# Kernel optimization log

Hardware: AMD Instinct MI355X
Metric: run time of the kernel (lower is better)

The kernel has to match this reference:

```python
import jax, jax.numpy as jnp
import numpy as np

B, T, N, F_IN, H, EV = 2, 12, 20000, 9, 64, 9
E = 200000


def setup_inputs() -> dict:
    key = jax.random.key(0)
    k = jax.random.split(key, 24)
    s = 0.1
    rn = lambda kk, shp: s * jax.random.normal(kk, shp, dtype=jnp.float32)
    d = {
        'graph_at_instance': jax.random.normal(k[0], (B, T, N, F_IN), dtype=jnp.float32),
        'target_event': jax.random.normal(k[1], (B, EV), dtype=jnp.float32),
        'input_event': jax.random.normal(k[2], (B, EV), dtype=jnp.float32),
        'edge_weight': jax.random.uniform(k[3], (E,), dtype=jnp.float32),
        'edge_src': jax.random.randint(k[4], (E,), 0, N, dtype=jnp.int32),
        'edge_dst': jax.random.randint(k[5], (E,), 0, N, dtype=jnp.int32),
        # 12 per-timestep GraphSAGE blocks (conv1: 9->64, conv2: 64->64, conv3: 64->9)
        'W1l': rn(k[6], (T, F_IN, H)), 'b1': jnp.zeros((T, H), jnp.float32), 'W1r': rn(k[7], (T, F_IN, H)),
        'W2l': rn(k[8], (T, H, H)),    'b2': jnp.zeros((T, H), jnp.float32), 'W2r': rn(k[9], (T, H, H)),
        'W3l': rn(k[10], (T, H, F_IN)),'b3': jnp.zeros((T, F_IN), jnp.float32), 'W3r': rn(k[11], (T, H, F_IN)),
        # 12 per-timestep GRU cells (9 -> 9), standard GRUCell parameterization
        'Wih': rn(k[12], (T, F_IN, 3 * F_IN)), 'Whh': rn(k[13], (T, F_IN, 3 * F_IN)),
        'bih': jnp.zeros((T, 3 * F_IN), jnp.float32), 'bhh': jnp.zeros((T, 3 * F_IN), jnp.float32),
        # encoder (18 -> 64) and decoder (64 -> 1)
        'enc_W': rn(k[14], (F_IN + EV, 64)), 'enc_b': jnp.zeros((64,), jnp.float32),
        'dec_W': rn(k[15], (64, 1)), 'dec_b': jnp.zeros((1,), jnp.float32),
    }
    return d


def _forward(graph_at_instance, target_event, input_event, edge_weight,
             W1l, b1, W1r, W2l, b2, W2r, W3l, b3, W3r,
             Wih, Whh, bih, bhh, enc_W, enc_b, dec_W, dec_b,
             edge_src, edge_dst):
    # in-degree for mean aggregation (clamped to avoid div by 0)
    deg = jnp.zeros((N,), jnp.float32).at[edge_dst].add(1.0)
    deg = jnp.maximum(deg, 1.0)[None, :, None]  # [1, N, 1]

    def sage(x, Wl, bl, Wr):
        # x: [B, N, d].  Weighted mean aggregation over edges, then lin_l(agg) + lin_r(x).
        m = x[:, edge_src] * edge_weight[None, :, None]          # [B, E, d]
        agg = jnp.zeros_like(x).at[:, edge_dst].add(m) / deg     # [B, N, d]
        return agg @ Wl + bl + x @ Wr

    def gru_cell(x, h, wih, whh, bih_t, bhh_t):
        gi = x @ wih + bih_t
        gh = h @ whh + bhh_t
        gir, giz, gin = jnp.split(gi, 3, axis=-1)
        ghr, ghz, ghn = jnp.split(gh, 3, axis=-1)
        r = jax.nn.sigmoid(gir + ghr)
        z = jax.nn.sigmoid(giz + ghz)
        n = jnp.tanh(gin + r * ghn)
        return (1.0 - z) * n + z * h

    def step(h, xs):
        xt, w1l, bb1, w1r, w2l, bb2, w2r, w3l, bb3, w3r, wih, whh, bih_t, bhh_t = xs
        x = jax.nn.elu(sage(xt, w1l, bb1, w1r))
        x = jax.nn.elu(sage(x, w2l, bb2, w2r))
        x = jax.nn.elu(sage(x, w3l, bb3, w3r))
        h = gru_cell(x, h, wih, whh, bih_t, bhh_t)
        return h, h

    xs = (jnp.swapaxes(graph_at_instance, 0, 1),  # [T, B, N, 9]
          W1l, b1, W1r, W2l, b2, W2r, W3l, b3, W3r, Wih, Whh, bih, bhh)
    h0 = jnp.zeros((B, N, F_IN), jnp.float32)
    _, outs = jax.lax.scan(step, h0, xs)          # [T, B, N, 9]
    outs = jnp.swapaxes(outs, 0, 1)               # [B, T, N, 9]

    te = jnp.broadcast_to(target_event[:, None, None, :], (B, T, N, EV))
    x = jnp.concatenate([outs, te], axis=-1)      # [B, T, N, 18]
    out = (x @ enc_W + enc_b) @ dec_W + dec_b     # [B, T, N, 1]
    mask = (graph_at_instance[..., 0:1] != 0).astype(out.dtype)
    return out * mask


def reference(graph_at_instance, target_event, input_event, edge_weight,
              W1l, b1, W1r, W2l, b2, W2r, W3l, b3, W3r,
              Wih, Whh, bih, bhh, enc_W, enc_b, dec_W, dec_b,
              edge_src, edge_dst):
    return _forward(graph_at_instance, target_event, input_event, edge_weight,
                    W1l, b1, W1r, W2l, b2, W2r, W3l, b3, W3r,
                    Wih, Whh, bih, bhh, enc_W, enc_b, dec_W, dec_b,
                    edge_src, edge_dst)
```

## Files before the change

### kernel.cpp

```cpp
#include <hip/hip_runtime.h>
#include <hip/hip_bf16.h>

#define BB 2
#define TT 12
#define NN 20000
#define FF 9
#define HH 64
#define EE 200000
#define NP 128

typedef __hip_bfloat16 bf;
typedef __attribute__((ext_vector_type(8))) short s8v;
typedef __attribute__((ext_vector_type(4))) float f4v;

__device__ unsigned g_xa[TT*NN*HH];
__device__ unsigned g_ag[TT*NN*HH];
__device__ unsigned g_xb[TT*NN*HH];
__device__ float2   g_x9[(size_t)NN*NP];
__device__ float2   g_xp[(size_t)NN*NP];
__device__ float2   g_z9[(size_t)NN*NP];
__device__ float2   g_r9[(size_t)NN*NP];
__device__ float2   g_a9[(size_t)NN*NP];
__device__ int      g_rp[NN+1];
__device__ int      g_cnt[NN];
__device__ int      g_csrc[EE];
__device__ float    g_cw[EE];
__device__ float    g_cvec[32];

__device__ __forceinline__ float lo2f(unsigned u){ unsigned v=u<<16; float f; __builtin_memcpy(&f,&v,4); return f; }
__device__ __forceinline__ float hi2f(unsigned u){ unsigned v=u&0xffff0000u; float f; __builtin_memcpy(&f,&v,4); return f; }
__device__ __forceinline__ unsigned short f2us(float f){ bf h=__float2bfloat16(f); unsigned short u; __builtin_memcpy(&u,&h,2); return u; }
__device__ __forceinline__ unsigned pack2(float a0, float a1){ return (unsigned)f2us(a0) | ((unsigned)f2us(a1)<<16); }
__device__ __forceinline__ float elu(float x){ return x>0.f ? x : expm1f(x); }

__global__ void k_zero(){
  int i = blockIdx.x*256 + threadIdx.x;
  if(i < NN) g_cnt[i] = 0;
}
__global__ void k_count(const int* __restrict__ dst){
  int e = blockIdx.x*256 + threadIdx.x;
  if(e < EE) atomicAdd(&g_cnt[dst[e]], 1);
}
__global__ void k_scan(){
  __shared__ int part[256];
  const int CH = 79;
  int t = threadIdx.x;
  int base = t*CH;
  int s = 0;
  for(int i=0;i<CH;i++){ int idx=base+i; if(idx<NN) s += g_cnt[idx]; }
  part[t] = s; __syncthreads();
  for(int off=1; off<256; off<<=1){
    int v = (t>=off) ? part[t-off] : 0;
    __syncthreads();
    part[t] += v;
    __syncthreads();
  }
  int run = (t==0) ? 0 : part[t-1];
  for(int i=0;i<CH;i++){
    int idx=base+i;
    if(idx<NN){ run += g_cnt[idx]; g_rp[idx+1] = run; }
  }
  if(t==0) g_rp[0] = 0;
}
__global__ void k_fill(const int* __restrict__ dst, const int* __restrict__ src,
                       const float* __restrict__ ew){
  int e = blockIdx.x*256 + threadIdx.x;
  if(e >= EE) return;
  int d = dst[e];
  int pos = g_rp[d] + atomicAdd(&g_cnt[d], 1);
  g_csrc[pos] = src[e];
  g_cw[pos]   = ew[e];
}

__global__ void k_head(const float* __restrict__ encW, const float* __restrict__ encb,
                       const float* __restrict__ decW, const float* __restrict__ decb,
                       const float* __restrict__ te){
  __shared__ float c[19];
  int tid = threadIdx.x;
  if(tid < 18){ float s=0.f; for(int j=0;j<64;j++) s += encW[tid*64+j]*decW[j]; c[tid]=s; }
  if(tid == 18){ float s=decb[0]; for(int j=0;j<64;j++) s += encb[j]*decW[j]; c[18]=s; }
  __syncthreads();
  if(tid < FF) g_cvec[tid] = c[tid];
  if(tid < BB){ float s=c[18]; for(int k=0;k<FF;k++) s += te[tid*FF+k]*c[9+k]; g_cvec[FF+tid]=s; }
}

__global__ void k_pack(const float* __restrict__ g){
  long i = (long)blockIdx.x*256 + threadIdx.x;
  if(i < (long)TT*NN*FF){
    int t = (int)(i / (NN*FF));
    int r = (int)(i - (long)t*NN*FF);
    int n = r / FF;
    int f = r - n*FF;
    float2 p;
    p.x = g[i];
    p.y = g[(long)TT*NN*FF + i];
    g_xp[(size_t)n*NP + t*FF + f] = p;
  }
}

__global__ void k_agg1(){
  int tid = threadIdx.x;
  int lane = tid & 63;
  int grp  = lane >> 4;
  int sub  = lane & 15;
  int wid = (blockIdx.x*256+tid)>>6, nw = gridDim.x*4;
  for(int n=wid; n<NN; n+=nw){
    int r0=g_rp[n], r1=g_rp[n+1];
    float inv = 1.f/fmaxf((float)(r1-r0), 1.f);
    float acc[16];
    #pragma unroll
    for(int s=0;s<16;s++) acc[s]=0.f;
    for(int base=r0; base<r1; base+=64){
      int cnt = min(64, r1-base);
      int ms = 0; float mw = 0.f;
      if(lane < cnt){ ms = g_csrc[base+lane]; mw = g_cw[base+lane]; }
      for(int k=0;k<cnt;k+=4){
        int   sg = __shfl(ms, k+grp, 64);
        float wg = __shfl(mw, k+grp, 64);
        const float4* p = reinterpret_cast<const float4*>(g_xp + (size_t)sg*NP) + sub*4;
        float4 v0=p[0], v1=p[1], v2=p[2], v3=p[3];
        acc[0]+=wg*v0.x; acc[1]+=wg*v0.y; acc[2]+=wg*v0.z; acc[3]+=wg*v0.w;
        acc[4]+=wg*v1.x; acc[5]+=wg*v1.y; acc[6]+=wg*v1.z; acc[7]+=wg*v1.w;
        acc[8]+=wg*v2.x; acc[9]+=wg*v2.y; acc[10]+=wg*v2.z; acc[11]+=wg*v2.w;
        acc[12]+=wg*v3.x; acc[13]+=wg*v3.y; acc[14]+=wg*v3.z; acc[15]+=wg*v3.w;
      }
    }
    #pragma unroll
    for(int s=0;s<16;s++){
      acc[s] += __shfl_xor(acc[s],16,64);
      acc[s] += __shfl_xor(acc[s],32,64);
    }
    if(grp == 0){
      float4* o = reinterpret_cast<float4*>(g_a9 + (size_t)n*NP) + sub*4;
      #pragma unroll
      for(int q=0;q<4;q++){
        float4 w;
        w.x = acc[q*4+0]*inv; w.y = acc[q*4+1]*inv;
        w.z = acc[q*4+2]*inv; w.w = acc[q*4+3]*inv;
        o[q] = w;
      }
    }
  }
}

__global__ __launch_bounds__(256) void k_gemm1(const float* __restrict__ Wl,
                                               const float* __restrict__ bias,
                                               const float* __restrict__ Wr){
  int t = blockIdx.y;
  __shared__ float sW[32*65];
  int tid = threadIdx.x;
  for(int i=tid; i<32*64; i+=256){
    int r = i >> 6, c = i & 63;
    float v = 0.f;
    if(r < FF)        v = Wl[(size_t)t*FF*HH + r*HH + c];
    else if(r < 2*FF) v = Wr[(size_t)t*FF*HH + (r-FF)*HH + c];
    sW[r*65+c] = v;
  }
  __syncthreads();
  int lane = tid & 63, wave = tid >> 6;
  int quad = lane >> 4, col = lane & 15;
  int base16 = blockIdx.x*64 + wave*16;
  if(base16 >= NN) return;
  size_t tb = (size_t)t*NN;
  int node = base16 + col;
  s8v A0, A1;
  #pragma unroll
  for(int j=0;j<8;j++){
    int k = quad*8 + j;
    float2 v = {0.f, 0.f};
    if(k < FF)        v = g_a9[(size_t)node*NP + t*FF + k];
    else if(k < 2*FF) v = g_xp[(size_t)node*NP + t*FF + (k-FF)];
    A0[j] = (short)f2us(v.x);
    A1[j] = (short)f2us(v.y);
  }
  #pragma unroll
  for(int nt=0; nt<4; nt++){
    f4v c0 = {0.f,0.f,0.f,0.f}, c1 = {0.f,0.f,0.f,0.f};
    s8v B;
    #pragma unroll
    for(int j=0;j<8;j++)
      B[j] = (short)f2us(sW[(quad*8+j)*65 + nt*16+col]);
    c0 = __builtin_amdgcn_mfma_f32_16x16x32_bf16(A0, B, c0, 0, 0, 0);
    c1 = __builtin_amdgcn_mfma_f32_16x16x32_bf16(A1, B, c1, 0, 0, 0);
    float bn = bias[t*HH + nt*16 + col];
    #pragma unroll
    for(int reg=0; reg<4; reg++){
      int nd = base16 + quad*4 + reg;
      g_xa[(tb+nd)*HH + nt*16 + col] = pack2(elu(c0[reg]+bn), elu(c1[reg]+bn));
    }
  }
}

__global__ void k_agg_all(){
  const unsigned* __restrict__ src = g_xa;
  int tid = threadIdx.x;
  int lane = tid & 63;
  int grp  = lane >> 4;
  int sub  = lane & 15;
  int wid = (blockIdx.x*256+tid)>>6, nw = gridDim.x*4;
  for(int idx=wid; idx<TT*NN; idx+=nw){
    unsigned ut = (unsigned)idx / NN;
    int n = idx - (int)(ut*NN);
    size_t tb = (size_t)ut*NN;
    const unsigned* __restrict__ rowp = src + tb*HH + (sub<<2);
    int r0=g_rp[n], r1=g_rp[n+1];
    float dg = fmaxf((float)(r1-r0), 1.f);
    float inv = 1.f/dg;
    float p0[4]={0.f,0.f,0.f,0.f}, p1[4]={0.f,0.f,0.f,0.f};
    for(int base=r0; base<r1; base+=64){
      int cnt = min(64, r1-base);
      int ms = 0; float mw = 0.f;
      if(lane < cnt){ ms = g_csrc[base+lane]; mw = g_cw[base+lane]; }
      for(int k=0;k<cnt;k+=4){
        int   sg = __shfl(ms, k+grp, 64);
        float wg = __shfl(mw, k+grp, 64);
        const uint4 v = *reinterpret_cast<const uint4*>(rowp + (size_t)sg*HH);
        p0[0]+=wg*lo2f(v.x); p1[0]+=wg*hi2f(v.x);
        p0[1]+=wg*lo2f(v.y); p1[1]+=wg*hi2f(v.y);
        p0[2]+=wg*lo2f(v.z); p1[2]+=wg*hi2f(v.z);
        p0[3]+=wg*lo2f(v.w); p1[3]+=wg*hi2f(v.w);
      }
    }
    #pragma unroll
    for(int q=0;q<4;q++){
      p0[q] += __shfl_xor(p0[q],16,64); p1[q] += __shfl_xor(p1[q],16,64);
      p0[q] += __shfl_xor(p0[q],32,64); p1[q] += __shfl_xor(p1[q],32,64);
    }
    if(lane < 16){
      uint4 o;
      o.x = pack2(p0[0]*inv, p1[0]*inv);
      o.y = pack2(p0[1]*inv, p1[1]*inv);
      o.z = pack2(p0[2]*inv, p1[2]*inv);
      o.w = pack2(p0[3]*inv, p1[3]*inv);
      *reinterpret_cast<uint4*>(g_ag + (tb + (size_t)n)*HH + (lane<<2)) = o;
    }
  }
}

__global__ __launch_bounds__(256) void k_gemm2_all(const float* __restrict__ Wl,
                                                   const float* __restrict__ bias,
                                                   const float* __restrict__ Wr){
  int t = blockIdx.y;
  __shared__ float sW[128*65];
  int tid = threadIdx.x;
  for(int i=tid; i<64*64; i+=256){
    int r = i >> 6, c = i & 63;
    sW[r*65+c]      = Wl[(size_t)t*4096 + i];
    sW[(r+64)*65+c] = Wr[(size_t)t*4096 + i];
  }
  __syncthreads();
  int lane = tid & 63, wave = tid >> 6;
  int quad = lane >> 4, col = lane & 15;
  int base16 = blockIdx.x*64 + wave*16;
  if(base16 >= NN) return;
  size_t tb = (size_t)t*NN;
  int nodeA = base16 + col;
  s8v A0[4], A1[4];
  #pragma unroll
  for(int ks=0; ks<4; ks++){
    const unsigned* srcb = (ks < 2) ? g_ag : g_xa;
    int koff = (ks & 1)*32 + quad*8;
    const uint4 u = *reinterpret_cast<const uint4*>(srcb + (tb+nodeA)*HH + koff);
    const uint4 v = *reinterpret_cast<const uint4*>(srcb + (tb+nodeA)*HH + koff + 4);
    unsigned uu[8] = {u.x,u.y,u.z,u.w,v.x,v.y,v.z,v.w};
    #pragma unroll
    for(int j=0;j<8;j++){
      A0[ks][j] = (short)(uu[j] & 0xffffu);
      A1[ks][j] = (short)(uu[j] >> 16);
    }
  }
  #pragma unroll
  for(int nt=0; nt<4; nt++){
    f4v c0 = {0.f,0.f,0.f,0.f}, c1 = {0.f,0.f,0.f,0.f};
    #pragma unroll
    for(int ks=0; ks<4; ks++){
      s8v B;
      #pragma unroll
      for(int j=0;j<8;j++)
        B[j] = (short)f2us(sW[(ks*32+quad*8+j)*65 + nt*16+col]);
      c0 = __builtin_amdgcn_mfma_f32_16x16x32_bf16(A0[ks], B, c0, 0, 0, 0);
      c1 = __builtin_amdgcn_mfma_f32_16x16x32_bf16(A1[ks], B, c1, 0, 0, 0);
    }
    float bn = bias[t*HH + nt*16 + col];
    #pragma unroll
    for(int reg=0; reg<4; reg++){
      int node = base16 + quad*4 + reg;
      g_xb[(tb+node)*HH + nt*16 + col] = pack2(elu(c0[reg]+bn), elu(c1[reg]+bn));
    }
  }
}

__global__ __launch_bounds__(256) void k_gemm3z(const float* __restrict__ Wl,
                                                const float* __restrict__ bias,
                                                const float* __restrict__ Wr){
  int t = blockIdx.y;
  __shared__ float sW[128*10];
  int tid = threadIdx.x;
  for(int i=tid; i<64*FF; i+=256){
    int r = i/FF, c = i - r*FF;
    sW[r*10+c]      = Wl[(size_t)t*HH*FF + i];
    sW[(r+64)*10+c] = Wr[(size_t)t*HH*FF + i];
  }
  __syncthreads();
  int lane = tid & 63, wave = tid >> 6;
  int quad = lane >> 4, col = lane & 15;
  int base16 = blockIdx.x*64 + wave*16;
  if(base16 >= NN) return;
  size_t tb = (size_t)t*NN;
  int nodeA = base16 + col;
  f4v z0={0.f,0.f,0.f,0.f}, z1={0.f,0.f,0.f,0.f};
  f4v r0={0.f,0.f,0.f,0.f}, r1={0.f,0.f,0.f,0.f};
  #pragma unroll
  for(int ks=0; ks<2; ks++){
    int koff = ks*32 + quad*8;
    const uint4 u = *reinterpret_cast<const uint4*>(g_xb + (tb+nodeA)*HH + koff);
    const uint4 v = *reinterpret_cast<const uint4*>(g_xb + (tb+nodeA)*HH + koff + 4);
    unsigned uu[8] = {u.x,u.y,u.z,u.w,v.x,v.y,v.z,v.w};
    s8v A0, A1, Bl, Br;
    #pragma unroll
    for(int j=0;j<8;j++){
      A0[j] = (short)(uu[j] & 0xffffu);
      A1[j] = (short)(uu[j] >> 16);
      int row = ks*32 + quad*8 + j;
      Bl[j] = (col < FF) ? (short)f2us(sW[row*10 + col])      : (short)0;
      Br[j] = (col < FF) ? (short)f2us(sW[(row+64)*10 + col]) : (short)0;
    }
    z0 = __builtin_amdgcn_mfma_f32_16x16x32_bf16(A0, Bl, z0, 0, 0, 0);
    z1 = __builtin_amdgcn_mfma_f32_16x16x32_bf16(A1, Bl, z1, 0, 0, 0);
    r0 = __builtin_amdgcn_mfma_f32_16x16x32_bf16(A0, Br, r0, 0, 0, 0);
    r1 = __builtin_amdgcn_mfma_f32_16x16x32_bf16(A1, Br, r1, 0, 0, 0);
  }
  if(col < FF){
    float bn = bias[t*FF + col];
    #pragma unroll
    for(int reg=0; reg<4; reg++){
      int node = base16 + quad*4 + reg;
      float2 oz; oz.x = z0[reg]; oz.y = z1[reg];
      float2 orr; orr.x = r0[reg]+bn; orr.y = r1[reg]+bn;
      g_z9[(size_t)node*NP + t*FF + col] = oz;
      g_r9[(size_t)node*NP + t*FF + col] = orr;
    }
  }
}

__global__ void k_agg9f(){
  int tid = threadIdx.x;
  int lane = tid & 63;
  int grp  = lane >> 4;
  int sub  = lane & 15;
  int wid = (blockIdx.x*256+tid)>>6, nw = gridDim.x*4;
  for(int n=wid; n<NN; n+=nw){
    int r0=g_rp[n], r1=g_rp[n+1];
    float inv = 1.f/fmaxf((float)(r1-r0), 1.f);
    float acc[16];
    #pragma unroll
    for(int s=0;s<16;s++) acc[s]=0.f;
    for(int base=r0; base<r1; base+=64){
      int cnt = min(64, r1-base);
      int ms = 0; float mw = 0.f;
      if(lane < cnt){ ms = g_csrc[base+lane]; mw = g_cw[base+lane]; }
      for(int k=0;k<cnt;k+=4){
        int   sg = __shfl(ms, k+grp, 64);
        float wg = __shfl(mw, k+grp, 64);
        const float4* p = reinterpret_cast<const float4*>(g_z9 + (size_t)sg*NP) + sub*4;
        float4 v0=p[0], v1=p[1], v2=p[2], v3=p[3];
        acc[0]+=wg*v0.x; acc[1]+=wg*v0.y; acc[2]+=wg*v0.z; acc[3]+=wg*v0.w;
        acc[4]+=wg*v1.x; acc[5]+=wg*v1.y; acc[6]+=wg*v1.z; acc[7]+=wg*v1.w;
        acc[8]+=wg*v2.x; acc[9]+=wg*v2.y; acc[10]+=wg*v2.z; acc[11]+=wg*v2.w;
        acc[12]+=wg*v3.x; acc[13]+=wg*v3.y; acc[14]+=wg*v3.z; acc[15]+=wg*v3.w;
      }
    }
    #pragma unroll
    for(int s=0;s<16;s++){
      acc[s] += __shfl_xor(acc[s],16,64);
      acc[s] += __shfl_xor(acc[s],32,64);
    }
    if(grp == 0){
      const float4* rp4 = reinterpret_cast<const float4*>(g_r9 + (size_t)n*NP) + sub*4;
      float4* o = reinterpret_cast<float4*>(g_x9 + (size_t)n*NP) + sub*4;
      #pragma unroll
      for(int q=0;q<4;q++){
        float4 r = rp4[q];
        float4 w;
        w.x = elu(acc[q*4+0]*inv + r.x);
        w.y = elu(acc[q*4+1]*inv + r.y);
        w.z = elu(acc[q*4+2]*inv + r.z);
        w.w = elu(acc[q*4+3]*inv + r.w);
        o[q] = w;
      }
    }
  }
}

__global__ __launch_bounds__(256) void k_gru_fused(const float* __restrict__ g,
                          const float* __restrict__ Wih, const float* __restrict__ Whh,
                          const float* __restrict__ bih, const float* __restrict__ bhh,
                          float* __restrict__ out){
  __shared__ float sWih[TT*FF*27];
  __shared__ float sWhh[TT*FF*27];
  __shared__ float sbih[TT*27], sbhh[TT*27];
  int tid = threadIdx.x;
  for(int i=tid;i<TT*FF*27;i+=256){ sWih[i]=Wih[i]; sWhh[i]=Whh[i]; }
  for(int i=tid;i<TT*27;i+=256){ sbih[i]=bih[i]; sbhh[i]=bhh[i]; }
  __syncthreads();
  int lane = tid & 63;
  int wv   = tid >> 6;
  int p    = lane / 9;
  int f    = lane - p*9;
  int gbase = p*9;
  int id = (blockIdx.x*4 + wv)*7 + p;
  bool valid = (p < 7) && (id < BB*NN);
  int b = 0, n = 0;
  if(valid){ b = (id >= NN) ? 1 : 0; n = id - b*NN; }
  float c9[FF];
  #pragma unroll
  for(int i=0;i<FF;i++) c9[i] = g_cvec[i];
  float cb = g_cvec[FF+b];
  float h = 0.f;
  float hs[FF];
  #pragma unroll
  for(int i=0;i<FF;i++) hs[i] = 0.f;
  for(int t=0;t<TT;t++){
    float x = 0.f;
    if(valid){
      float2 xf = g_x9[(size_t)n*NP + t*FF + f];
      x = b ? xf.y : xf.x;
    }
    float xs[FF];
    #pragma unroll
    for(int i=0;i<FF;i++) xs[i] = __shfl(x, gbase+i, 64);
    const float* wi = &sWih[t*FF*27];
    const float* wh = &sWhh[t*FF*27];
    float gir = sbih[t*27+f], giz = sbih[t*27+9+f], gin = sbih[t*27+18+f];
    float ghr = sbhh[t*27+f], ghz = sbhh[t*27+9+f], ghn = sbhh[t*27+18+f];
    #pragma unroll
    for(int i=0;i<FF;i++){
      float xi = xs[i], hi = hs[i];
      gir += xi*wi[i*27+f];    giz += xi*wi[i*27+9+f];    gin += xi*wi[i*27+18+f];
      ghr += hi*wh[i*27+f];    ghz += hi*wh[i*27+9+f];    ghn += hi*wh[i*27+18+f];
    }
    float r = 1.f/(1.f+__expf(-(gir+ghr)));
    float z = 1.f/(1.f+__expf(-(giz+ghz)));
    float nv = tanhf(gin + r*ghn);
    h = (1.f-z)*nv + z*h;
    #pragma unroll
    for(int i=0;i<FF;i++) hs[i] = __shfl(h, gbase+i, 64);
    if(valid && f == 0){
      float acc = cb;
      #pragma unroll
      for(int i=0;i<FF;i++) acc += hs[i]*c9[i];
      size_t gidx = (size_t)(b*TT+t)*NN + n;
      float m = (g[gidx*FF] != 0.f) ? 1.f : 0.f;
      out[gidx] = acc*m;
    }
  }
}

extern "C" void kernel_launch(void* const* d_in, const int* in_sizes, int n_in,
                              void* d_out, int out_size, void* d_ws, size_t ws_size,
                              hipStream_t stream){
  const float* g    = (const float*)d_in[0];
  const float* te   = (const float*)d_in[1];
  const float* ew   = (const float*)d_in[3];
  const int* esrc = (const int*)d_in[4];
  const int* edst = (const int*)d_in[5];
  const float* W1l=(const float*)d_in[6];  const float* b1 =(const float*)d_in[7];  const float* W1r=(const float*)d_in[8];
  const float* W2l=(const float*)d_in[9];  const float* b2 =(const float*)d_in[10]; const float* W2r=(const float*)d_in[11];
  const float* W3l=(const float*)d_in[12]; const float* b3 =(const float*)d_in[13]; const float* W3r=(const float*)d_in[14];
  const float* Wih=(const float*)d_in[15]; const float* Whh=(const float*)d_in[16];
  const float* bih=(const float*)d_in[17]; const float* bhh=(const float*)d_in[18];
  const float* encW=(const float*)d_in[19]; const float* encb=(const float*)d_in[20];
  const float* decW=(const float*)d_in[21]; const float* decb=(const float*)d_in[22];
  float* out = (float*)d_out;

  k_zero <<<(NN+255)/256, 256, 0, stream>>>();
  k_count<<<(EE+255)/256, 256, 0, stream>>>(edst);
  k_scan <<<1, 256, 0, stream>>>();
  k_zero <<<(NN+255)/256, 256, 0, stream>>>();
  k_fill <<<(EE+255)/256, 256, 0, stream>>>(edst, esrc, ew);
  k_head <<<1, 64, 0, stream>>>(encW, encb, decW, decb, te);
  k_pack <<<((long)TT*NN*FF+255)/256, 256, 0, stream>>>(g);

  dim3 ggm((NN+63)/64, TT);
  k_agg1<<<2048, 256, 0, stream>>>();
  k_gemm1<<<ggm, 256, 0, stream>>>(W1l, b1, W1r);
  k_agg_all<<<2048, 256, 0, stream>>>();
  k_gemm2_all<<<ggm, 256, 0, stream>>>(W2l, b2, W2r);
  k_gemm3z<<<ggm, 256, 0, stream>>>(W3l, b3, W3r);
  k_agg9f<<<2048, 256, 0, stream>>>();
  int nblk = (BB*NN + 27) / 28;
  k_gru_fused<<<nblk, 256, 0, stream>>>(g, Wih, Whh, bih, bhh, out);
}
```

Measured before the change: 540.0 us.

## Fuse conv2 and conv3 GEMMs via LDS, merge setup kernels, store bf16 weights

Combines the conv2 and conv3 GEMM kernels into one, keeping each wave's conv2 output tile in shared memory instead of writing and rereading a global intermediate buffer. The head-constant computation and the second count-zeroing are folded into the scan kernel, cutting three launches. Weights are converted to bf16 once when staged into shared memory rather than on every B-fragment read. The fused kernel uses more LDS per block (about 37 KB), which may reduce occupancy.

```diff
diff --git a/kernel.cpp b/kernel.cpp
--- a/kernel.cpp
+++ b/kernel.cpp
@@ -15,7 +15,6 @@
 
 __device__ unsigned g_xa[TT*NN*HH];
 __device__ unsigned g_ag[TT*NN*HH];
-__device__ unsigned g_xb[TT*NN*HH];
 __device__ float2   g_x9[(size_t)NN*NP];
 __device__ float2   g_xp[(size_t)NN*NP];
 __device__ float2   g_z9[(size_t)NN*NP];
@@ -41,8 +40,11 @@
   int e = blockIdx.x*256 + threadIdx.x;
   if(e < EE) atomicAdd(&g_cnt[dst[e]], 1);
 }
-__global__ void k_scan(){
+__global__ void k_scan(const float* __restrict__ encW, const float* __restrict__ encb,
+                       const float* __restrict__ decW, const float* __restrict__ decb,
+                       const float* __restrict__ te){
   __shared__ int part[256];
+  __shared__ float c[19];
   const int CH = 79;
   int t = threadIdx.x;
   int base = t*CH;
@@ -58,9 +60,14 @@
   int run = (t==0) ? 0 : part[t-1];
   for(int i=0;i<CH;i++){
     int idx=base+i;
-    if(idx<NN){ run += g_cnt[idx]; g_rp[idx+1] = run; }
+    if(idx<NN){ run += g_cnt[idx]; g_rp[idx+1] = run; g_cnt[idx] = 0; }
   }
   if(t==0) g_rp[0] = 0;
+  if(t < 18){ float v=0.f; for(int j=0;j<64;j++) v += encW[t*64+j]*decW[j]; c[t]=v; }
+  if(t == 18){ float v=decb[0]; for(int j=0;j<64;j++) v += encb[j]*decW[j]; c[18]=v; }
+  __syncthreads();
+  if(t < FF) g_cvec[t] = c[t];
+  if(t < BB){ float v=c[18]; for(int k=0;k<FF;k++) v += te[t*FF+k]*c[9+k]; g_cvec[FF+t]=v; }
 }
 __global__ void k_fill(const int* __restrict__ dst, const int* __restrict__ src,
                        const float* __restrict__ ew){
@@ -70,18 +77,6 @@
   int pos = g_rp[d] + atomicAdd(&g_cnt[d], 1);
   g_csrc[pos] = src[e];
   g_cw[pos]   = ew[e];
-}
-
-__global__ void k_head(const float* __restrict__ encW, const float* __restrict__ encb,
-                       const float* __restrict__ decW, const float* __restrict__ decb,
-                       const float* __restrict__ te){
-  __shared__ float c[19];
-  int tid = threadIdx.x;
-  if(tid < 18){ float s=0.f; for(int j=0;j<64;j++) s += encW[tid*64+j]*decW[j]; c[tid]=s; }
-  if(tid == 18){ float s=decb[0]; for(int j=0;j<64;j++) s += encb[j]*decW[j]; c[18]=s; }
-  __syncthreads();
-  if(tid < FF) g_cvec[tid] = c[tid];
-  if(tid < BB){ float s=c[18]; for(int k=0;k<FF;k++) s += te[tid*FF+k]*c[9+k]; g_cvec[FF+tid]=s; }
 }
 
 __global__ void k_pack(const float* __restrict__ g){
@@ -147,14 +142,14 @@
                                                const float* __restrict__ bias,
                                                const float* __restrict__ Wr){
   int t = blockIdx.y;
-  __shared__ float sW[32*65];
+  __shared__ unsigned short sW[32*65];
   int tid = threadIdx.x;
   for(int i=tid; i<32*64; i+=256){
     int r = i >> 6, c = i & 63;
     float v = 0.f;
     if(r < FF)        v = Wl[(size_t)t*FF*HH + r*HH + c];
     else if(r < 2*FF) v = Wr[(size_t)t*FF*HH + (r-FF)*HH + c];
-    sW[r*65+c] = v;
+    sW[r*65+c] = f2us(v);
   }
   __syncthreads();
   int lane = tid & 63, wave = tid >> 6;
@@ -179,7 +174,7 @@
     s8v B;
     #pragma unroll
     for(int j=0;j<8;j++)
-      B[j] = (short)f2us(sW[(quad*8+j)*65 + nt*16+col]);
+      B[j] = (short)sW[(quad*8+j)*65 + nt*16+col];
     c0 = __builtin_amdgcn_mfma_f32_16x16x32_bf16(A0, B, c0, 0, 0, 0);
     c1 = __builtin_amdgcn_mfma_f32_16x16x32_bf16(A1, B, c1, 0, 0, 0);
     float bn = bias[t*HH + nt*16 + col];
@@ -237,16 +232,26 @@
   }
 }
 
-__global__ __launch_bounds__(256) void k_gemm2_all(const float* __restrict__ Wl,
-                                                   const float* __restrict__ bias,
-                                                   const float* __restrict__ Wr){
+__global__ __launch_bounds__(256) void k_gemm23(const float* __restrict__ W2l,
+                                                const float* __restrict__ b2,
+                                                const float* __restrict__ W2r,
+                                                const float* __restrict__ W3l,
+                                                const float* __restrict__ b3,
+                                                const float* __restrict__ W3r){
   int t = blockIdx.y;
-  __shared__ float sW[128*65];
+  __shared__ unsigned short sW2[128*65];
+  __shared__ unsigned short sW3[128*10];
+  __shared__ unsigned sXB[64*66];
   int tid = threadIdx.x;
   for(int i=tid; i<64*64; i+=256){
     int r = i >> 6, c = i & 63;
-    sW[r*65+c]      = Wl[(size_t)t*4096 + i];
-    sW[(r+64)*65+c] = Wr[(size_t)t*4096 + i];
+    sW2[r*65+c]      = f2us(W2l[(size_t)t*4096 + i]);
+    sW2[(r+64)*65+c] = f2us(W2r[(size_t)t*4096 + i]);
+  }
+  for(int i=tid; i<64*FF; i+=256){
+    int r = i/FF, c = i - r*FF;
+    sW3[r*10+c]      = f2us(W3l[(size_t)t*HH*FF + i]);
+    sW3[(r+64)*10+c] = f2us(W3r[(size_t)t*HH*FF + i]);
   }
   __syncthreads();
   int lane = tid & 63, wave = tid >> 6;
@@ -254,91 +259,74 @@
   int base16 = blockIdx.x*64 + wave*16;
   if(base16 >= NN) return;
   size_t tb = (size_t)t*NN;
-  int nodeA = base16 + col;
-  s8v A0[4], A1[4];
-  #pragma unroll
-  for(int ks=0; ks<4; ks++){
-    const unsigned* srcb = (ks < 2) ? g_ag : g_xa;
-    int koff = (ks & 1)*32 + quad*8;
-    const uint4 u = *reinterpret_cast<const uint4*>(srcb + (tb+nodeA)*HH + koff);
-    const uint4 v = *reinterpret_cast<const uint4*>(srcb + (tb+nodeA)*HH + koff + 4);
-    unsigned uu[8] = {u.x,u.y,u.z,u.w,v.x,v.y,v.z,v.w};
-    #pragma unroll
-    for(int j=0;j<8;j++){
-      A0[ks][j] = (short)(uu[j] & 0xffffu);
-      A1[ks][j] = (short)(uu[j] >> 16);
-    }
-  }
-  #pragma unroll
-  for(int nt=0; nt<4; nt++){
-    f4v c0 = {0.f,0.f,0.f,0.f}, c1 = {0.f,0.f,0.f,0.f};
+  {
+    int nodeA = base16 + col;
+    s8v A0[4], A1[4];
     #pragma unroll
     for(int ks=0; ks<4; ks++){
-      s8v B;
-      #pragma unroll
-      for(int j=0;j<8;j++)
-        B[j] = (short)f2us(sW[(ks*32+quad*8+j)*65 + nt*16+col]);
-      c0 = __builtin_amdgcn_mfma_f32_16x16x32_bf16(A0[ks], B, c0, 0, 0, 0);
-      c1 = __builtin_amdgcn_mfma_f32_16x16x32_bf16(A1[ks], B, c1, 0, 0, 0);
-    }
-    float bn = bias[t*HH + nt*16 + col];
-    #pragma unroll
-    for(int reg=0; reg<4; reg++){
-      int node = base16 + quad*4 + reg;
-      g_xb[(tb+node)*HH + nt*16 + col] = pack2(elu(c0[reg]+bn), elu(c1[reg]+bn));
-    }
-  }
-}
-
-__global__ __launch_bounds__(256) void k_gemm3z(const float* __restrict__ Wl,
-                                                const float* __restrict__ bias,
-                                                const float* __restrict__ Wr){
-  int t = blockIdx.y;
-  __shared__ float sW[128*10];
-  int tid = threadIdx.x;
-  for(int i=tid; i<64*FF; i+=256){
-    int r = i/FF, c = i - r*FF;
-    sW[r*10+c]      = Wl[(size_t)t*HH*FF + i];
-    sW[(r+64)*10+c] = Wr[(size_t)t*HH*FF + i];
-  }
-  __syncthreads();
-  int lane = tid & 63, wave = tid >> 6;
-  int quad = lane >> 4, col = lane & 15;
-  int base16 = blockIdx.x*64 + wave*16;
-  if(base16 >= NN) return;
-  size_t tb = (size_t)t*NN;
-  int nodeA = base16 + col;
-  f4v z0={0.f,0.f,0.f,0.f}, z1={0.f,0.f,0.f,0.f};
-  f4v r0={0.f,0.f,0.f,0.f}, r1={0.f,0.f,0.f,0.f};
-  #pragma unroll
-  for(int ks=0; ks<2; ks++){
-    int koff = ks*32 + quad*8;
-    const uint4 u = *reinterpret_cast<const uint4*>(g_xb + (tb+nodeA)*HH + koff);
-    const uint4 v = *reinterpret_cast<const uint4*>(g_xb + (tb+nodeA)*HH + koff + 4);
-    unsigned uu[8] = {u.x,u.y,u.z,u.w,v.x,v.y,v.z,v.w};
-    s8v A0, A1, Bl, Br;
-    #pragma unroll
-    for(int j=0;j<8;j++){
-      A0[j] = (short)(uu[j] & 0xffffu);
-      A1[j] = (short)(uu[j] >> 16);
-      int row = ks*32 + quad*8 + j;
-      Bl[j] = (col < FF) ? (short)f2us(sW[row*10 + col])      : (short)0;
-      Br[j] = (col < FF) ? (short)f2us(sW[(row+64)*10 + col]) : (short)0;
-    }
-    z0 = __builtin_amdgcn_mfma_f32_16x16x32_bf16(A0, Bl, z0, 0, 0, 0);
-    z1 = __builtin_amdgcn_mfma_f32_16x16x32_bf16(A1, Bl, z1, 0, 0, 0);
-    r0 = __builtin_amdgcn_mfma_f32_16x16x32_bf16(A0, Br, r0, 0, 0, 0);
-    r1 = __builtin_amdgcn_mfma_f32_16x16x32_bf16(A1, Br, r1, 0, 0, 0);
-  }
-  if(col < FF){
-    float bn = bias[t*FF + col];
-    #pragma unroll
-    for(int reg=0; reg<4; reg++){
-      int node = base16 + quad*4 + reg;
-      float2 oz; oz.x = z0[reg]; oz.y = z1[reg];
-      float2 orr; orr.x = r0[reg]+bn; orr.y = r1[reg]+bn;
-      g_z9[(size_t)node*NP + t*FF + col] = oz;
-      g_r9[(size_t)node*NP + t*FF + col] = orr;
+      const unsigned* srcb = (ks < 2) ? g_ag : g_xa;
+      int koff = (ks & 1)*32 + quad*8;
+      const uint4 u = *reinterpret_cast<const uint4*>(srcb + (tb+nodeA)*HH + koff);
+      const uint4 v = *reinterpret_cast<const uint4*>(srcb + (tb+nodeA)*HH + koff + 4);
+      unsigned uu[8] = {u.x,u.y,u.z,u.w,v.x,v.y,v.z,v.w};
+      #pragma unroll
+      for(int j=0;j<8;j++){
+        A0[ks][j] = (short)(uu[j] & 0xffffu);
+        A1[ks][j] = (short)(uu[j] >> 16);
+      }
+    }
+    #pragma unroll
+    for(int nt=0; nt<4; nt++){
+      f4v c0 = {0.f,0.f,0.f,0.f}, c1 = {0.f,0.f,0.f,0.f};
+      #pragma unroll
+      for(int ks=0; ks<4; ks++){
+        s8v B;
+        #pragma unroll
+        for(int j=0;j<8;j++)
+          B[j] = (short)sW2[(ks*32+quad*8+j)*65 + nt*16+col];
+        c0 = __builtin_amdgcn_mfma_f32_16x16x32_bf16(A0[ks], B, c0, 0, 0, 0);
+        c1 = __builtin_amdgcn_mfma_f32_16x16x32_bf16(A1[ks], B, c1, 0, 0, 0);
+      }
+      float bn = b2[t*HH + nt*16 + col];
+      #pragma unroll
+      for(int reg=0; reg<4; reg++){
+        int nl = wave*16 + quad*4 + reg;
+        sXB[nl*66 + nt*16 + col] = pack2(elu(c0[reg]+bn), elu(c1[reg]+bn));
+      }
+    }
+  }
+  {
+    f4v z0={0.f,0.f,0.f,0.f}, z1={0.f,0.f,0.f,0.f};
+    f4v r0={0.f,0.f,0.f,0.f}, r1={0.f,0.f,0.f,0.f};
+    int nlA = wave*16 + col;
+    #pragma unroll
+    for(int ks=0; ks<2; ks++){
+      int koff = ks*32 + quad*8;
+      s8v A0, A1, Bl, Br;
+      #pragma unroll
+      for(int j=0;j<8;j++){
+        unsigned u = sXB[nlA*66 + koff + j];
+        A0[j] = (short)(u & 0xffffu);
+        A1[j] = (short)(u >> 16);
+        int row = ks*32 + quad*8 + j;
+        Bl[j] = (col < FF) ? (short)sW3[row*10 + col]      : (short)0;
+        Br[j] = (col < FF) ? (short)sW3[(row+64)*10 + col] : (short)0;
+      }
+      z0 = __builtin_amdgcn_mfma_f32_16x16x32_bf16(A0, Bl, z0, 0, 0, 0);
+      z1 = __builtin_amdgcn_mfma_f32_16x16x32_bf16(A1, Bl, z1, 0, 0, 0);
+      r0 = __builtin_amdgcn_mfma_f32_16x16x32_bf16(A0, Br, r0, 0, 0, 0);
+      r1 = __builtin_amdgcn_mfma_f32_16x16x32_bf16(A1, Br, r1, 0, 0, 0);
+    }
+    if(col < FF){
+      float bn = b3[t*FF + col];
+      #pragma unroll
+      for(int reg=0; reg<4; reg++){
+        int node = base16 + quad*4 + reg;
+        float2 oz; oz.x = z0[reg]; oz.y = z1[reg];
+        float2 orr; orr.x = r0[reg]+bn; orr.y = r1[reg]+bn;
+        g_z9[(size_t)node*NP + t*FF + col] = oz;
+        g_r9[(size_t)node*NP + t*FF + col] = orr;
+      }
     }
   }
 }
@@ -475,18 +463,15 @@
 
   k_zero <<<(NN+255)/256, 256, 0, stream>>>();
   k_count<<<(EE+255)/256, 256, 0, stream>>>(edst);
-  k_scan <<<1, 256, 0, stream>>>();
-  k_zero <<<(NN+255)/256, 256, 0, stream>>>();
+  k_scan <<<1, 256, 0, stream>>>(encW, encb, decW, decb, te);
   k_fill <<<(EE+255)/256, 256, 0, stream>>>(edst, esrc, ew);
-  k_head <<<1, 64, 0, stream>>>(encW, encb, decW, decb, te);
   k_pack <<<((long)TT*NN*FF+255)/256, 256, 0, stream>>>(g);
 
   dim3 ggm((NN+63)/64, TT);
   k_agg1<<<2048, 256, 0, stream>>>();
   k_gemm1<<<ggm, 256, 0, stream>>>(W1l, b1, W1r);
   k_agg_all<<<2048, 256, 0, stream>>>();
-  k_gemm2_all<<<ggm, 256, 0, stream>>>(W2l, b2, W2r);
-  k_gemm3z<<<ggm, 256, 0, stream>>>(W3l, b3, W3r);
+  k_gemm23<<<ggm, 256, 0, stream>>>(W2l, b2, W2r, W3l, b3, W3r);
   k_agg9f<<<2048, 256, 0, stream>>>();
   int nblk = (BB*NN + 27) / 28;
   k_gru_fused<<<nblk, 256, 0, stream>>>(g, Wih, Whh, bih, bhh, out);
```

Result: no change. 531.1 us (-1.6%).
